# Kernel optimization log

Hardware: AMD Instinct MI355X
Metric: run time of the kernel (lower is better)

The kernel has to match this reference:

```python
import jax, jax.numpy as jnp
import numpy as np

D_MODEL = 1024
N_HEADS = 16
HEAD_DIM = D_MODEL // N_HEADS
BATCH = 4
SEQ = 2048
NEG_INF = -1000000000.0  # matches torch masked_fill value in source


def setup_inputs() -> dict:
    key = jax.random.key(0)
    ks = jax.random.split(key, 5)
    scale = 1.0 / np.sqrt(D_MODEL)
    x = jax.random.normal(ks[0], (BATCH, SEQ, D_MODEL), dtype=jnp.float32)
    wq = jax.random.normal(ks[1], (D_MODEL, D_MODEL), dtype=jnp.float32) * scale
    wk = jax.random.normal(ks[2], (D_MODEL, D_MODEL), dtype=jnp.float32) * scale
    wv = jax.random.normal(ks[3], (D_MODEL, D_MODEL), dtype=jnp.float32) * scale
    wo = jax.random.normal(ks[4], (D_MODEL, D_MODEL), dtype=jnp.float32) * scale
    return {"x": x, "wq": wq, "wk": wk, "wv": wv, "wo": wo}


def reference(x, wq, wk, wv, wo):
    b, s, d = x.shape
    # projections (weights applied as x @ W^T, matching nn-style Linear weights)
    q = jnp.einsum('bsd,ed->bse', x, wq).reshape(b, s, N_HEADS, HEAD_DIM).transpose(0, 2, 1, 3)
    k = jnp.einsum('bsd,ed->bse', x, wk).reshape(b, s, N_HEADS, HEAD_DIM).transpose(0, 2, 1, 3)
    v = jnp.einsum('bsd,ed->bse', x, wv).reshape(b, s, N_HEADS, HEAD_DIM).transpose(0, 2, 1, 3)
    # scaled dot-product scores [b, h, s, s]
    scores = jnp.einsum('bhqd,bhkd->bhqk', q, k) / jnp.sqrt(jnp.float32(HEAD_DIM))
    # causal mask: positions strictly above diagonal masked with -1e9
    causal = jnp.triu(jnp.ones((s, s), dtype=bool), k=1)
    scores = jnp.where(causal[None, None], jnp.float32(NEG_INF), scores)
    attn = jax.nn.softmax(scores, axis=-1)
    out = jnp.einsum('bhqk,bhkd->bhqd', attn, v)
    out = out.transpose(0, 2, 1, 3).reshape(b, s, d)
    return jnp.einsum('bsd,ed->bse', out, wo)
```

## Files before the change

kernel.cpp:

```cpp
#include <hip/hip_runtime.h>
#include <hip/hip_bf16.h>

typedef __hip_bfloat16 bf16;
typedef __attribute__((ext_vector_type(8))) short short8;
typedef __attribute__((ext_vector_type(4))) short short4_t;
typedef __attribute__((ext_vector_type(4))) float f32x4;
typedef unsigned int u32;

#define MFMA16(a, b, c) __builtin_amdgcn_mfma_f32_16x16x32_bf16(a, b, c, 0, 0, 0)

static constexpr int S_ = 2048, D_ = 1024, M_ = 8192;

__device__ __forceinline__ void gload16(void* lds, const void* g) {
  __builtin_amdgcn_global_load_lds((const __attribute__((address_space(1))) void*)g,
                                   (__attribute__((address_space(3))) void*)lds, 16, 0, 0);
}

__device__ __forceinline__ short4_t cvt4(const float4 v) {
  short4_t r;
  r[0] = (short)__bfloat16_as_ushort(__float2bfloat16(v.x));
  r[1] = (short)__bfloat16_as_ushort(__float2bfloat16(v.y));
  r[2] = (short)__bfloat16_as_ushort(__float2bfloat16(v.z));
  r[3] = (short)__bfloat16_as_ushort(__float2bfloat16(v.w));
  return r;
}

__device__ __forceinline__ u32 pk2(float a, float b) {
  return (u32)__bfloat16_as_ushort(__float2bfloat16(a)) |
         ((u32)__bfloat16_as_ushort(__float2bfloat16(b)) << 16);
}

__global__ __launch_bounds__(256) void cvt_f32_bf16(const float* __restrict__ in,
                                                    bf16* __restrict__ out, int n4) {
  int stride = gridDim.x * 256;
  for (int i = blockIdx.x * 256 + threadIdx.x; i < n4; i += stride) {
    float4 v = ((const float4*)in)[i];
    *(short4_t*)&out[(size_t)i * 4] = cvt4(v);
  }
}

template <int MODE, class TC>
__global__ __launch_bounds__(256) void gemm_bt(const bf16* __restrict__ A,
                                               const bf16* __restrict__ W,
                                               TC* __restrict__ C, float scale) {
  __shared__ __align__(16) bf16 lA[128 * 32];
  __shared__ __align__(16) bf16 lB[128 * 32];
  const int tid = threadIdx.x, lane = tid & 63, w = tid >> 6;
  const int wr = w >> 1, wc = w & 1;
  const int m0 = blockIdx.x * 128, n0 = blockIdx.y * 128;
  const int l15 = lane & 15, lg = lane >> 4;

  f32x4 zero = {0.f, 0.f, 0.f, 0.f};
  f32x4 acc[4][4];
#pragma unroll
  for (int i = 0; i < 4; i++)
#pragma unroll
    for (int j = 0; j < 4; j++) acc[i][j] = zero;

  for (int kt = 0; kt < 32; ++kt) {
    const int k0 = kt * 32;
#pragma unroll
    for (int i = 0; i < 2; ++i) {
      int c = i * 256 + tid;
      int row = c >> 2, col = (c & 3) * 8;
      gload16(&lA[c * 8], &A[(size_t)(m0 + row) * 1024 + k0 + col]);
      gload16(&lB[c * 8], &W[(size_t)(n0 + row) * 1024 + k0 + col]);
    }
    __syncthreads();

    short8 af[4], bfr[4];
#pragma unroll
    for (int mi = 0; mi < 4; mi++)
      af[mi] = *(const short8*)&lA[(wr * 64 + mi * 16 + l15) * 32 + lg * 8];
#pragma unroll
    for (int ni = 0; ni < 4; ni++)
      bfr[ni] = *(const short8*)&lB[(wc * 64 + ni * 16 + l15) * 32 + lg * 8];
#pragma unroll
    for (int mi = 0; mi < 4; mi++)
#pragma unroll
      for (int ni = 0; ni < 4; ni++) acc[mi][ni] = MFMA16(af[mi], bfr[ni], acc[mi][ni]);
    __syncthreads();
  }

#pragma unroll
  for (int mi = 0; mi < 4; mi++)
#pragma unroll
    for (int ni = 0; ni < 4; ni++)
#pragma unroll
      for (int r = 0; r < 4; r++) {
        int m = m0 + wr * 64 + mi * 16 + lg * 4 + r;
        int n = n0 + wc * 64 + ni * 16 + l15;
        float v = acc[mi][ni][r] * scale;
        size_t idx;
        if constexpr (MODE == 0) {
          idx = (size_t)m * 1024 + n;
        } else {
          int b = m >> 11, s = m & 2047, h = n >> 6, dh = n & 63;
          if constexpr (MODE == 1)
            idx = ((size_t)((b << 4) + h) * 2048 + s) * 64 + dh;
          else
            idx = ((size_t)((b << 4) + h) * 64 + dh) * 2048 + s;
        }
        if constexpr (sizeof(TC) == 4)
          C[idx] = v;
        else
          C[idx] = __float2bfloat16(v);
      }
}

__global__ __launch_bounds__(256, 3) void attn_fwd(const bf16* __restrict__ Q,
                                                   const bf16* __restrict__ K,
                                                   const bf16* __restrict__ Vt,
                                                   bf16* __restrict__ O) {
  __shared__ __align__(16) bf16 lK[2][64 * 64];
  __shared__ __align__(16) bf16 lV[2][64 * 64];
  __shared__ __align__(16) bf16 lP[4][32 * 64];
  const int tid = threadIdx.x, lane = tid & 63, w = tid >> 6;
  const int l15 = lane & 15, lg = lane >> 4;
  const int bh = blockIdx.x;
  const int qb = 15 - blockIdx.y;
  const int q0 = qb * 128 + w * 32;
  const bf16* Qb = Q + (size_t)bh * S_ * 64;
  const bf16* Kb = K + (size_t)bh * S_ * 64;
  const bf16* Vb = Vt + (size_t)bh * 64 * S_;
  bf16* Pw = lP[w];

  short8 qf[2][2];
#pragma unroll
  for (int mi = 0; mi < 2; mi++)
#pragma unroll
    for (int kd = 0; kd < 2; kd++)
      qf[mi][kd] = *(const short8*)&Qb[(size_t)(q0 + mi * 16 + l15) * 64 + kd * 32 + lg * 8];

  f32x4 zero = {0.f, 0.f, 0.f, 0.f};
  f32x4 acc[2][4];
  float mr[2], lr[2];
#pragma unroll
  for (int mi = 0; mi < 2; mi++) {
    mr[mi] = -1e9f;
    lr[mi] = 0.f;
#pragma unroll
    for (int ni = 0; ni < 4; ni++) acc[mi][ni] = zero;
  }

  const int nch = (qb + 1) * 2;

#define STAGE(buf, c)                                                                   \
  {                                                                                     \
    _Pragma("unroll") for (int i = 0; i < 2; ++i) {                                     \
      int t2 = i * 256 + tid;                                                           \
      int row = t2 >> 3;                                                                \
      int cb = ((t2 & 7) * 16) ^ ((row & 7) << 4);                                      \
      gload16((char*)lK[buf] + t2 * 16, (const char*)Kb + (size_t)((c) * 64 + row) * 128 + cb); \
      gload16((char*)lV[buf] + t2 * 16, (const char*)Vb + (size_t)row * 4096 + (size_t)(c) * 128 + cb); \
    }                                                                                   \
  }

  STAGE(0, 0);
  int cur = 0;
  for (int c = 0; c < nch; ++c) {
    __builtin_amdgcn_s_barrier();
    if (c + 1 < nch) {
      STAGE(cur ^ 1, c + 1);
      asm volatile("s_waitcnt vmcnt(4)" ::: "memory");
    } else {
      asm volatile("s_waitcnt vmcnt(0)" ::: "memory");
    }
    __builtin_amdgcn_s_barrier();

    if (c * 64 <= q0 + 31) {
      const int c0 = c * 64;
      f32x4 sc[2][4];
#pragma unroll
      for (int mi = 0; mi < 2; mi++)
#pragma unroll
        for (int ch = 0; ch < 4; ch++) sc[mi][ch] = zero;
      const char* Kc = (const char*)lK[cur];
      __builtin_amdgcn_s_setprio(1);
#pragma unroll
      for (int kd = 0; kd < 2; ++kd)
#pragma unroll
        for (int ch = 0; ch < 4; ++ch) {
          short8 kf = *(const short8*)(Kc + (ch * 16 + l15) * 128 + ((kd * 64 + lg * 16) ^ ((l15 & 7) << 4)));
          sc[0][ch] = MFMA16(kf, qf[0][kd], sc[0][ch]);
          sc[1][ch] = MFMA16(kf, qf[1][kd], sc[1][ch]);
        }
      __builtin_amdgcn_s_setprio(0);

      if (c0 + 63 > q0) {
#pragma unroll
        for (int mi = 0; mi < 2; mi++) {
          int q = q0 + mi * 16 + l15;
#pragma unroll
          for (int ch = 0; ch < 4; ch++)
#pragma unroll
            for (int r = 0; r < 4; r++) {
              int kv = c0 + ch * 16 + lg * 4 + r;
              if (kv > q) sc[mi][ch][r] = -1e9f;
            }
        }
      }

#pragma unroll
      for (int mi = 0; mi < 2; mi++) {
        float v01 = fmaxf(fmaxf(sc[mi][0][0], sc[mi][0][1]), fmaxf(sc[mi][0][2], sc[mi][0][3]));
        float v1 = fmaxf(fmaxf(sc[mi][1][0], sc[mi][1][1]), fmaxf(sc[mi][1][2], sc[mi][1][3]));
        float v2 = fmaxf(fmaxf(sc[mi][2][0], sc[mi][2][1]), fmaxf(sc[mi][2][2], sc[mi][2][3]));
        float v3 = fmaxf(fmaxf(sc[mi][3][0], sc[mi][3][1]), fmaxf(sc[mi][3][2], sc[mi][3][3]));
        float vmax = fmaxf(fmaxf(v01, v1), fmaxf(v2, v3));
        vmax = fmaxf(vmax, __shfl_xor(vmax, 16));
        vmax = fmaxf(vmax, __shfl_xor(vmax, 32));
        float mn = fmaxf(mr[mi], vmax);
        float corr = __expf(mr[mi] - mn);
        mr[mi] = mn;
        float ps = 0.f;
#pragma unroll
        for (int ch = 0; ch < 4; ch++)
#pragma unroll
          for (int r = 0; r < 4; r++) {
            float p = __expf(sc[mi][ch][r] - mn);
            sc[mi][ch][r] = p;
            ps += p;
          }
        ps += __shfl_xor(ps, 16);
        ps += __shfl_xor(ps, 32);
        lr[mi] = lr[mi] * corr + ps;
#pragma unroll
        for (int r = 0; r < 4; r++) {
          float cr = __shfl(corr, (lane & 48) | (((lane >> 4) << 2) + r));
#pragma unroll
          for (int ni = 0; ni < 4; ni++) acc[mi][ni][r] *= cr;
        }
        int row = mi * 16 + l15;
        char* Pb = (char*)Pw + row * 128;
        int sw = (row & 7) << 4;
#pragma unroll
        for (int ch = 0; ch < 4; ch++) {
          u32 d0 = pk2(sc[mi][ch][0], sc[mi][ch][1]);
          u32 d1 = pk2(sc[mi][ch][2], sc[mi][ch][3]);
          uint2 dd = {d0, d1};
          *(uint2*)(Pb + ((ch * 32 + lg * 8) ^ sw)) = dd;
        }
      }

      asm volatile("s_waitcnt lgkmcnt(0)" ::: "memory");
      const char* Vc = (const char*)lV[cur];
      __builtin_amdgcn_s_setprio(1);
#pragma unroll
      for (int kd = 0; kd < 2; ++kd) {
        short8 pf[2];
#pragma unroll
        for (int mi = 0; mi < 2; mi++)
          pf[mi] = *(const short8*)((const char*)Pw + (mi * 16 + l15) * 128 +
                                    ((kd * 64 + lg * 16) ^ ((l15 & 7) << 4)));
#pragma unroll
        for (int ni = 0; ni < 4; ++ni) {
          short8 vf = *(const short8*)(Vc + (ni * 16 + l15) * 128 + ((kd * 64 + lg * 16) ^ ((l15 & 7) << 4)));
          acc[0][ni] = MFMA16(pf[0], vf, acc[0][ni]);
          acc[1][ni] = MFMA16(pf[1], vf, acc[1][ni]);
        }
      }
      __builtin_amdgcn_s_setprio(0);
    }
    cur ^= 1;
  }
#undef STAGE

  const int b = bh >> 4, h = bh & 15;
#pragma unroll
  for (int mi = 0; mi < 2; mi++) {
    float lrr[4];
#pragma unroll
    for (int r = 0; r < 4; r++)
      lrr[r] = __shfl(lr[mi], (lane & 48) | (((lane >> 4) << 2) + r));
#pragma unroll
    for (int ni = 0; ni < 4; ni++)
#pragma unroll
      for (int r = 0; r < 4; r++) {
        int q = q0 + mi * 16 + lg * 4 + r;
        size_t idx = ((size_t)(b * 2048 + q)) * 1024 + h * 64 + ni * 16 + l15;
        O[idx] = __float2bfloat16(acc[mi][ni][r] / lrr[r]);
      }
  }
}

extern "C" void kernel_launch(void* const* d_in, const int* in_sizes, int n_in,
                              void* d_out, int out_size, void* d_ws, size_t ws_size,
                              hipStream_t stream) {
  const float* x = (const float*)d_in[0];
  const float* wq = (const float*)d_in[1];
  const float* wk = (const float*)d_in[2];
  const float* wv = (const float*)d_in[3];
  const float* wo = (const float*)d_in[4];
  float* out = (float*)d_out;

  const size_t SZ = (size_t)M_ * D_;
  const size_t WSZ = (size_t)D_ * D_;
  bf16* xb = (bf16*)d_ws;
  bf16* Qw = xb + SZ;
  bf16* Kw = Qw + SZ;
  bf16* Vw = Kw + SZ;
  bf16* AO = xb;
  bf16* wqb = (bf16*)d_out;
  bf16* wkb = wqb + WSZ;
  bf16* wvb = wkb + WSZ;
  bf16* wob = Qw;

  dim3 blk(256), grid(64, 8);
  hipLaunchKernelGGL(cvt_f32_bf16, dim3(2048), blk, 0, stream, x, xb, (int)(SZ / 4));
  hipLaunchKernelGGL(cvt_f32_bf16, dim3(1024), blk, 0, stream, wq, wqb, (int)(WSZ / 4));
  hipLaunchKernelGGL(cvt_f32_bf16, dim3(1024), blk, 0, stream, wk, wkb, (int)(WSZ / 4));
  hipLaunchKernelGGL(cvt_f32_bf16, dim3(1024), blk, 0, stream, wv, wvb, (int)(WSZ / 4));
  hipLaunchKernelGGL((gemm_bt<1, bf16>), grid, blk, 0, stream, xb, wqb, Qw, 0.125f);
  hipLaunchKernelGGL((gemm_bt<1, bf16>), grid, blk, 0, stream, xb, wkb, Kw, 1.0f);
  hipLaunchKernelGGL((gemm_bt<2, bf16>), grid, blk, 0, stream, xb, wvb, Vw, 1.0f);
  hipLaunchKernelGGL(attn_fwd, dim3(64, 16), blk, 0, stream, Qw, Kw, Vw, AO);
  hipLaunchKernelGGL(cvt_f32_bf16, dim3(1024), blk, 0, stream, wo, wob, (int)(WSZ / 4));
  hipLaunchKernelGGL((gemm_bt<0, float>), grid, blk, 0, stream, AO, wob, out, 1.0f);
}
```

Measured before the change: 277.4 us.

## Fuse QKV projections and weight conversions, use exp2 softmax with lazy rescale

Merges the three weight conversion kernels (and the wo conversion, when the workspace is large enough) into one launch, and the three Q/K/V projection GEMMs into a single launch with a 1536-block grid. The log2(e) factor is folded into the Q scale so the attention softmax can use exp2f. The running max and output rescale are now skipped unless some row's max grows by more than 8. This cuts launch count and tail effects and removes per-tile rescaling work, at the cost of values growing up to 2^8 before rescale.

After: 281.8 us. About the same (+1.6%).

```diff
diff --git a/kernel.cpp b/kernel.cpp
--- a/kernel.cpp
+++ b/kernel.cpp
@@ -10,6 +10,9 @@
 #define MFMA16(a, b, c) __builtin_amdgcn_mfma_f32_16x16x32_bf16(a, b, c, 0, 0, 0)
 
 static constexpr int S_ = 2048, D_ = 1024, M_ = 8192;
+static constexpr size_t SZ = (size_t)M_ * D_;
+static constexpr size_t WSZ = (size_t)D_ * D_;
+static constexpr float QSCALE = 0.125f * 1.4426950408889634f;
 
 __device__ __forceinline__ void gload16(void* lds, const void* g) {
   __builtin_amdgcn_global_load_lds((const __attribute__((address_space(1))) void*)g,
@@ -39,15 +42,31 @@
   }
 }
 
-template <int MODE, class TC>
-__global__ __launch_bounds__(256) void gemm_bt(const bf16* __restrict__ A,
-                                               const bf16* __restrict__ W,
-                                               TC* __restrict__ C, float scale) {
+__global__ __launch_bounds__(256) void cvt_w(const float* __restrict__ s0, const float* __restrict__ s1,
+                                             const float* __restrict__ s2, const float* __restrict__ s3,
+                                             bf16* __restrict__ dqkv, bf16* __restrict__ dwo, int nseg) {
+  const int per = 1 << 18;
+  int total = nseg * per;
+  for (int i = blockIdx.x * 256 + threadIdx.x; i < total; i += gridDim.x * 256) {
+    int seg = i >> 18, off = i & (per - 1);
+    const float* s = (seg == 0) ? s0 : (seg == 1) ? s1 : (seg == 2) ? s2 : s3;
+    bf16* d = (seg < 3) ? (dqkv + ((size_t)seg << 20)) : dwo;
+    float4 v = ((const float4*)s)[off];
+    *(short4_t*)&d[(size_t)off * 4] = cvt4(v);
+  }
+}
+
+__global__ __launch_bounds__(256) void qkv_gemm(const bf16* __restrict__ A,
+                                                const bf16* __restrict__ Wqkv,
+                                                bf16* __restrict__ QKV) {
   __shared__ __align__(16) bf16 lA[128 * 32];
   __shared__ __align__(16) bf16 lB[128 * 32];
   const int tid = threadIdx.x, lane = tid & 63, w = tid >> 6;
   const int wr = w >> 1, wc = w & 1;
-  const int m0 = blockIdx.x * 128, n0 = blockIdx.y * 128;
+  const int m0 = blockIdx.x * 128;
+  const int mat = blockIdx.y >> 3, n0 = (blockIdx.y & 7) * 128;
+  const bf16* W = Wqkv + (size_t)mat * WSZ;
+  bf16* C = QKV + (size_t)mat * SZ;
   const int l15 = lane & 15, lg = lane >> 4;
 
   f32x4 zero = {0.f, 0.f, 0.f, 0.f};
@@ -82,6 +101,7 @@
     __syncthreads();
   }
 
+  const float scale = (mat == 0) ? QSCALE : 1.0f;
 #pragma unroll
   for (int mi = 0; mi < 4; mi++)
 #pragma unroll
@@ -90,21 +110,64 @@
       for (int r = 0; r < 4; r++) {
         int m = m0 + wr * 64 + mi * 16 + lg * 4 + r;
         int n = n0 + wc * 64 + ni * 16 + l15;
-        float v = acc[mi][ni][r] * scale;
-        size_t idx;
-        if constexpr (MODE == 0) {
-          idx = (size_t)m * 1024 + n;
-        } else {
-          int b = m >> 11, s = m & 2047, h = n >> 6, dh = n & 63;
-          if constexpr (MODE == 1)
-            idx = ((size_t)((b << 4) + h) * 2048 + s) * 64 + dh;
-          else
-            idx = ((size_t)((b << 4) + h) * 64 + dh) * 2048 + s;
-        }
-        if constexpr (sizeof(TC) == 4)
-          C[idx] = v;
-        else
-          C[idx] = __float2bfloat16(v);
+        int b = m >> 11, s = m & 2047, h = n >> 6, dh = n & 63;
+        size_t idx = (mat < 2) ? (((size_t)((b << 4) + h) * 2048 + s) * 64 + dh)
+                               : (((size_t)((b << 4) + h) * 64 + dh) * 2048 + s);
+        C[idx] = __float2bfloat16(acc[mi][ni][r] * scale);
+      }
+}
+
+__global__ __launch_bounds__(256) void gemm_out(const bf16* __restrict__ A,
+                                                const bf16* __restrict__ W,
+                                                float* __restrict__ C) {
+  __shared__ __align__(16) bf16 lA[128 * 32];
+  __shared__ __align__(16) bf16 lB[128 * 32];
+  const int tid = threadIdx.x, lane = tid & 63, w = tid >> 6;
+  const int wr = w >> 1, wc = w & 1;
+  const int m0 = blockIdx.x * 128, n0 = blockIdx.y * 128;
+  const int l15 = lane & 15, lg = lane >> 4;
+
+  f32x4 zero = {0.f, 0.f, 0.f, 0.f};
+  f32x4 acc[4][4];
+#pragma unroll
+  for (int i = 0; i < 4; i++)
+#pragma unroll
+    for (int j = 0; j < 4; j++) acc[i][j] = zero;
+
+  for (int kt = 0; kt < 32; ++kt) {
+    const int k0 = kt * 32;
+#pragma unroll
+    for (int i = 0; i < 2; ++i) {
+      int c = i * 256 + tid;
+      int row = c >> 2, col = (c & 3) * 8;
+      gload16(&lA[c * 8], &A[(size_t)(m0 + row) * 1024 + k0 + col]);
+      gload16(&lB[c * 8], &W[(size_t)(n0 + row) * 1024 + k0 + col]);
+    }
+    __syncthreads();
+
+    short8 af[4], bfr[4];
+#pragma unroll
+    for (int mi = 0; mi < 4; mi++)
+      af[mi] = *(const short8*)&lA[(wr * 64 + mi * 16 + l15) * 32 + lg * 8];
+#pragma unroll
+    for (int ni = 0; ni < 4; ni++)
+      bfr[ni] = *(const short8*)&lB[(wc * 64 + ni * 16 + l15) * 32 + lg * 8];
+#pragma unroll
+    for (int mi = 0; mi < 4; mi++)
+#pragma unroll
+      for (int ni = 0; ni < 4; ni++) acc[mi][ni] = MFMA16(af[mi], bfr[ni], acc[mi][ni]);
+    __syncthreads();
+  }
+
+#pragma unroll
+  for (int mi = 0; mi < 4; mi++)
+#pragma unroll
+    for (int ni = 0; ni < 4; ni++)
+#pragma unroll
+      for (int r = 0; r < 4; r++) {
+        int m = m0 + wr * 64 + mi * 16 + lg * 4 + r;
+        int n = n0 + wc * 64 + ni * 16 + l15;
+        C[(size_t)m * 1024 + n] = acc[mi][ni][r];
       }
 }
 
@@ -203,34 +266,37 @@
 
 #pragma unroll
       for (int mi = 0; mi < 2; mi++) {
-        float v01 = fmaxf(fmaxf(sc[mi][0][0], sc[mi][0][1]), fmaxf(sc[mi][0][2], sc[mi][0][3]));
+        float v0 = fmaxf(fmaxf(sc[mi][0][0], sc[mi][0][1]), fmaxf(sc[mi][0][2], sc[mi][0][3]));
         float v1 = fmaxf(fmaxf(sc[mi][1][0], sc[mi][1][1]), fmaxf(sc[mi][1][2], sc[mi][1][3]));
         float v2 = fmaxf(fmaxf(sc[mi][2][0], sc[mi][2][1]), fmaxf(sc[mi][2][2], sc[mi][2][3]));
         float v3 = fmaxf(fmaxf(sc[mi][3][0], sc[mi][3][1]), fmaxf(sc[mi][3][2], sc[mi][3][3]));
-        float vmax = fmaxf(fmaxf(v01, v1), fmaxf(v2, v3));
+        float vmax = fmaxf(fmaxf(v0, v1), fmaxf(v2, v3));
         vmax = fmaxf(vmax, __shfl_xor(vmax, 16));
         vmax = fmaxf(vmax, __shfl_xor(vmax, 32));
-        float mn = fmaxf(mr[mi], vmax);
-        float corr = __expf(mr[mi] - mn);
-        mr[mi] = mn;
+        if (!__all(vmax <= mr[mi] + 8.f)) {
+          float mn = fmaxf(mr[mi], vmax);
+          float corr = exp2f(mr[mi] - mn);
+          mr[mi] = mn;
+          lr[mi] *= corr;
+#pragma unroll
+          for (int r = 0; r < 4; r++) {
+            float cr = __shfl(corr, (lane & 48) | (((lane >> 4) << 2) + r));
+#pragma unroll
+            for (int ni = 0; ni < 4; ni++) acc[mi][ni][r] *= cr;
+          }
+        }
         float ps = 0.f;
 #pragma unroll
         for (int ch = 0; ch < 4; ch++)
 #pragma unroll
           for (int r = 0; r < 4; r++) {
-            float p = __expf(sc[mi][ch][r] - mn);
+            float p = exp2f(sc[mi][ch][r] - mr[mi]);
             sc[mi][ch][r] = p;
             ps += p;
           }
         ps += __shfl_xor(ps, 16);
         ps += __shfl_xor(ps, 32);
-        lr[mi] = lr[mi] * corr + ps;
-#pragma unroll
-        for (int r = 0; r < 4; r++) {
-          float cr = __shfl(corr, (lane & 48) | (((lane >> 4) << 2) + r));
-#pragma unroll
-          for (int ni = 0; ni < 4; ni++) acc[mi][ni][r] *= cr;
-        }
+        lr[mi] += ps;
         int row = mi * 16 + l15;
         char* Pb = (char*)Pw + row * 128;
         int sw = (row & 7) << 4;
@@ -294,27 +360,21 @@
   const float* wo = (const float*)d_in[4];
   float* out = (float*)d_out;
 
-  const size_t SZ = (size_t)M_ * D_;
-  const size_t WSZ = (size_t)D_ * D_;
   bf16* xb = (bf16*)d_ws;
   bf16* Qw = xb + SZ;
-  bf16* Kw = Qw + SZ;
-  bf16* Vw = Kw + SZ;
   bf16* AO = xb;
-  bf16* wqb = (bf16*)d_out;
-  bf16* wkb = wqb + WSZ;
-  bf16* wvb = wkb + WSZ;
-  bf16* wob = Qw;
-
-  dim3 blk(256), grid(64, 8);
+  bf16* wqkv = (bf16*)d_out;
+
+  const bool ws_has_wo = ws_size >= (4 * SZ + WSZ) * sizeof(bf16);
+  bf16* wob = ws_has_wo ? (xb + 4 * SZ) : Qw;
+
+  dim3 blk(256);
   hipLaunchKernelGGL(cvt_f32_bf16, dim3(2048), blk, 0, stream, x, xb, (int)(SZ / 4));
-  hipLaunchKernelGGL(cvt_f32_bf16, dim3(1024), blk, 0, stream, wq, wqb, (int)(WSZ / 4));
-  hipLaunchKernelGGL(cvt_f32_bf16, dim3(1024), blk, 0, stream, wk, wkb, (int)(WSZ / 4));
-  hipLaunchKernelGGL(cvt_f32_bf16, dim3(1024), blk, 0, stream, wv, wvb, (int)(WSZ / 4));
-  hipLaunchKernelGGL((gemm_bt<1, bf16>), grid, blk, 0, stream, xb, wqb, Qw, 0.125f);
-  hipLaunchKernelGGL((gemm_bt<1, bf16>), grid, blk, 0, stream, xb, wkb, Kw, 1.0f);
-  hipLaunchKernelGGL((gemm_bt<2, bf16>), grid, blk, 0, stream, xb, wvb, Vw, 1.0f);
-  hipLaunchKernelGGL(attn_fwd, dim3(64, 16), blk, 0, stream, Qw, Kw, Vw, AO);
-  hipLaunchKernelGGL(cvt_f32_bf16, dim3(1024), blk, 0, stream, wo, wob, (int)(WSZ / 4));
-  hipLaunchKernelGGL((gemm_bt<0, float>), grid, blk, 0, stream, AO, wob, out, 1.0f);
-}
+  hipLaunchKernelGGL(cvt_w, dim3(1024), blk, 0, stream, wq, wk, wv, wo, wqkv, wob,
+                     ws_has_wo ? 4 : 3);
+  hipLaunchKernelGGL(qkv_gemm, dim3(64, 24), blk, 0, stream, xb, wqkv, Qw);
+  hipLaunchKernelGGL(attn_fwd, dim3(64, 16), blk, 0, stream, Qw, Qw + SZ, Qw + 2 * SZ, AO);
+  if (!ws_has_wo)
+    hipLaunchKernelGGL(cvt_f32_bf16, dim3(512), blk, 0, stream, wo, wob, (int)(WSZ / 4));
+  hipLaunchKernelGGL(gemm_out, dim3(64, 8), blk, 0, stream, AO, wob, out);
+}
```
